# Kernel optimization log

Measured on AMD Instinct MI355X. Metric: run time of the kernel, lower is better.

## Reference

```python
import jax, jax.numpy as jnp
import numpy as np

D_MODEL = 512
NHEAD = 8
DIM = D_MODEL // NHEAD
EPS_ATT = 1e-6
EPS_LN = 1e-5


def layer_norm(x, gamma, beta):
    mu = jnp.mean(x, axis=-1, keepdims=True)
    var = jnp.mean(jnp.square(x - mu), axis=-1, keepdims=True)
    return (x - mu) * jax.lax.rsqrt(var + EPS_LN) * gamma + beta


def setup_inputs() -> dict:
    key = jax.random.key(0)
    ks = jax.random.split(key, 12)
    B, L = 4, 4096
    s = 1.0 / np.sqrt(D_MODEL)
    inp = {
        "q": jax.random.normal(ks[0], (B, L, D_MODEL), jnp.float32),
        "k": jax.random.normal(ks[1], (B, L, D_MODEL), jnp.float32),
        "v": jax.random.normal(ks[2], (B, L, D_MODEL), jnp.float32),
        # weights stored [in, out] so application is x @ W (== torch Linear with W.T)
        "Wq": jax.random.normal(ks[3], (D_MODEL, D_MODEL), jnp.float32) * s,
        "Wk": jax.random.normal(ks[4], (D_MODEL, D_MODEL), jnp.float32) * s,
        "Wv": jax.random.normal(ks[5], (D_MODEL, D_MODEL), jnp.float32) * s,
        "Wm": jax.random.normal(ks[6], (D_MODEL, D_MODEL), jnp.float32) * s,
        "W1": jax.random.normal(ks[7], (D_MODEL, 4 * D_MODEL), jnp.float32) * s,
        "W2": jax.random.normal(ks[8], (4 * D_MODEL, D_MODEL), jnp.float32) * (0.5 * s),
        "g1": jnp.ones((D_MODEL,), jnp.float32),
        "b1": jnp.zeros((D_MODEL,), jnp.float32),
        "g2": jnp.ones((D_MODEL,), jnp.float32),
        "b2": jnp.zeros((D_MODEL,), jnp.float32),
    }
    return inp


def reference(q, k, v, Wq, Wk, Wv, Wm, W1, W2, g1, b1, g2, b2):
    B, L, _ = q.shape
    S = k.shape[1]
    # projections -> [B, L, H, D]
    Qp = (q @ Wq).reshape(B, L, NHEAD, DIM)
    Kp = (k @ Wk).reshape(B, S, NHEAD, DIM)
    Vp = (v @ Wv).reshape(B, S, NHEAD, DIM)
    # elu+1 feature map linear attention
    Q = jax.nn.elu(Qp) + 1.0
    K = jax.nn.elu(Kp) + 1.0
    Vn = Vp / S
    KV = jnp.einsum('nshd,nshv->nhdv', K, Vn)          # [B,H,D,D]
    Z = 1.0 / (jnp.einsum('nlhd,nhd->nlh', Q, K.sum(axis=1)) + EPS_ATT)
    msg = jnp.einsum('nlhd,nhdv,nlh->nlhv', Q, KV, Z) * S  # [B,L,H,D]
    # merge + residual + norm1
    msg = msg.reshape(B, L, D_MODEL) @ Wm
    msg = layer_norm(msg + q, g1, b1)
    # FFN; note original adds mlp output to q (not norm1 output)
    ffn = jax.nn.relu(msg @ W1) @ W2
    out = layer_norm(q + ffn, g2, b2)
    return out
```

## Files before the change

kernel.cpp:

```cpp
#include <hip/hip_runtime.h>

typedef unsigned short u16;
typedef unsigned int u32;

typedef __bf16 bf16x8 __attribute__((ext_vector_type(8)));
typedef float f32x4 __attribute__((ext_vector_type(4)));

#define EPI_BF16 0
#define EPI_ELU1 1
#define EPI_RELU 2
#define EPI_ADDRES_F32 3
#define EPI_PROJ3 4

__device__ __forceinline__ float bf2f(u16 x) {
    u32 u = ((u32)x) << 16;
    return __uint_as_float(u);
}
__device__ __forceinline__ u16 f2bf(float f) {
    u32 u = __float_as_uint(f);
    u32 r = (u + 0x7FFFu + ((u >> 16) & 1u)) >> 16;
    return (u16)r;
}

__device__ __forceinline__ void gload_lds16(const u16* g, u16* l) {
    __builtin_amdgcn_global_load_lds(
        (const __attribute__((address_space(1))) u32*)g,
        (__attribute__((address_space(3))) u32*)l, 16, 0, 0);
}

__global__ __launch_bounds__(256) void f2b3_k(
    const float* __restrict__ q, const float* __restrict__ k,
    const float* __restrict__ v, u16* __restrict__ out) {
    int bid = blockIdx.x;
    int w = bid >> 13;
    const float* in = (w == 0) ? q : (w == 1) ? k : v;
    int i = ((bid & 8191) * 256 + threadIdx.x) * 4;
    float4 f = *(const float4*)(in + i);
    ushort4 o;
    o.x = f2bf(f.x); o.y = f2bf(f.y); o.z = f2bf(f.z); o.w = f2bf(f.w);
    *(ushort4*)(out + (long)w * 8388608 + i) = o;
}

__global__ __launch_bounds__(256) void transpose4_k(
    const float* __restrict__ W0, const float* __restrict__ W1,
    const float* __restrict__ W2, const float* __restrict__ W3,
    u16* __restrict__ out) {
    int idx = blockIdx.x * 256 + threadIdx.x;
    int w = idx >> 18, local = idx & 262143;
    const float* in = (w == 0) ? W0 : (w == 1) ? W1 : (w == 2) ? W2 : W3;
    int c = local >> 9, r = local & 511;
    out[idx] = f2bf(in[r * 512 + c]);
}

__global__ __launch_bounds__(256) void transpose2_k(
    const float* __restrict__ W1, const float* __restrict__ W2,
    u16* __restrict__ out) {
    int idx = blockIdx.x * 256 + threadIdx.x;
    if (idx < 1048576) {
        int c = idx / 512, r = idx % 512;
        out[idx] = f2bf(W1[(long)r * 2048 + c]);
    } else {
        int local = idx - 1048576;
        int c = local / 2048, r = local % 2048;
        out[idx] = f2bf(W2[(long)r * 512 + c]);
    }
}

__global__ __launch_bounds__(256) void gemm_bt(
    const u16* __restrict__ A, const u16* __restrict__ Bt,
    void* __restrict__ C, const float* __restrict__ Res,
    int M, int N, int K, int epi)
{
    __shared__ __align__(16) u16 As[2][4096];
    __shared__ __align__(16) u16 Bs[2][4096];

    int t = threadIdx.x;
    int gx = gridDim.x;
    int nwg = gx * gridDim.y;
    int bid = blockIdx.y * gx + blockIdx.x;
    if ((nwg & 7) == 0) {
        int cpx = nwg >> 3;
        bid = (bid & 7) * cpx + (bid >> 3);
    }
    int m0 = (bid / gx) * 128, n0 = (bid % gx) * 128;

    int third = 0;
    if (epi == EPI_PROJ3) {
        third = n0 >> 9;
        A += (long)third * 8388608;
    }

    int wave = t >> 6, lane = t & 63;
    int wm = (wave >> 1) * 64, wn = (wave & 1) * 64;
    int lrow = lane & 15, lk8 = (lane >> 4) * 8;

    f32x4 acc[4][4] = {};

    int srow = wave * 16 + (lane >> 2);
    int scol = (lane & 3) * 8;
    const u16* pA0 = A + (long)(m0 + srow) * K + scol;
    const u16* pB0 = Bt + (long)(n0 + srow) * K + scol;
    const long s64 = (long)64 * K;

    int nt = K >> 5;
    int cur = 0;

    {
        u16* a = As[0] + wave * 512;
        u16* b = Bs[0] + wave * 512;
        gload_lds16(pA0, a);
        gload_lds16(pA0 + s64, a + 2048);
        gload_lds16(pB0, b);
        gload_lds16(pB0 + s64, b + 2048);
    }
    __builtin_amdgcn_s_waitcnt(0);
    __syncthreads();

    for (int kt = 0; kt < nt; ++kt) {
        if (kt + 1 < nt) {
            int k0 = (kt + 1) << 5;
            u16* a = As[cur ^ 1] + wave * 512;
            u16* b = Bs[cur ^ 1] + wave * 512;
            gload_lds16(pA0 + k0, a);
            gload_lds16(pA0 + s64 + k0, a + 2048);
            gload_lds16(pB0 + k0, b);
            gload_lds16(pB0 + s64 + k0, b + 2048);
        }

        const u16* As_c = As[cur];
        const u16* Bs_c = Bs[cur];
        bf16x8 af[4], bfr[4];
#pragma unroll
        for (int mi = 0; mi < 4; mi++)
            af[mi] = *(const bf16x8*)(As_c + (wm + mi * 16 + lrow) * 32 + lk8);
#pragma unroll
        for (int ni = 0; ni < 4; ni++)
            bfr[ni] = *(const bf16x8*)(Bs_c + (wn + ni * 16 + lrow) * 32 + lk8);
#pragma unroll
        for (int mi = 0; mi < 4; mi++)
#pragma unroll
            for (int ni = 0; ni < 4; ni++)
                acc[mi][ni] = __builtin_amdgcn_mfma_f32_16x16x32_bf16(
                    af[mi], bfr[ni], acc[mi][ni], 0, 0, 0);

        if (kt + 1 < nt) {
            __builtin_amdgcn_s_waitcnt(0);
            __syncthreads();
            cur ^= 1;
        }
    }

    int rq = (lane >> 4) * 4;
    int colb = n0 + wn + (lane & 15);
#pragma unroll
    for (int mi = 0; mi < 4; mi++) {
#pragma unroll
        for (int ni = 0; ni < 4; ni++) {
#pragma unroll
            for (int r = 0; r < 4; r++) {
                int row = m0 + wm + mi * 16 + rq + r;
                int col = colb + ni * 16;
                float v0 = acc[mi][ni][r];
                if (epi == EPI_PROJ3) {
                    u16* Cb = (u16*)C + (long)third * 8388608;
                    long idx = (long)row * 512 + (col - (third << 9));
                    float v = (third < 2)
                                  ? (v0 > 0.f ? v0 + 1.f : __expf(v0))
                                  : v0;
                    Cb[idx] = f2bf(v);
                } else {
                    long idx = (long)row * N + col;
                    if (epi == EPI_ELU1) {
                        float v = v0 > 0.f ? v0 + 1.f : __expf(v0);
                        ((u16*)C)[idx] = f2bf(v);
                    } else if (epi == EPI_RELU) {
                        ((u16*)C)[idx] = f2bf(v0 > 0.f ? v0 : 0.f);
                    } else if (epi == EPI_ADDRES_F32) {
                        ((float*)C)[idx] = v0 + Res[idx];
                    } else {
                        ((u16*)C)[idx] = f2bf(v0);
                    }
                }
            }
        }
    }
}

__global__ __launch_bounds__(256) void gemm_bt64(
    const u16* __restrict__ A, const u16* __restrict__ Bt,
    void* __restrict__ C, const float* __restrict__ Res,
    int M, int N, int K, int epi)
{
    __shared__ __align__(16) u16 As[2][8192];
    __shared__ __align__(16) u16 Bs[2][8192];

    int t = threadIdx.x;
    int gx = gridDim.x;
    int nwg = gx * gridDim.y;
    int bid = blockIdx.y * gx + blockIdx.x;
    if ((nwg & 7) == 0) {
        int cpx = nwg >> 3;
        bid = (bid & 7) * cpx + (bid >> 3);
    }
    int m0 = (bid / gx) * 128, n0 = (bid % gx) * 128;

    int wave = t >> 6, lane = t & 63;
    int wm = (wave >> 1) * 64, wn = (wave & 1) * 64;
    int lrow = lane & 15, lk8 = (lane >> 4) * 8;

    f32x4 acc[4][4] = {};

    int srow = wave * 16 + (lane >> 2);
    int scol = (lane & 3) * 8;
    const u16* pA0 = A + (long)(m0 + srow) * K + scol;
    const u16* pB0 = Bt + (long)(n0 + srow) * K + scol;
    const long s64 = (long)64 * K;

    int nt = K >> 6;
    int cur = 0;

    {
        u16* a = As[0] + wave * 512;
        u16* b = Bs[0] + wave * 512;
#pragma unroll
        for (int kk = 0; kk < 2; kk++) {
            gload_lds16(pA0 + kk * 32, a + kk * 4096);
            gload_lds16(pA0 + s64 + kk * 32, a + kk * 4096 + 2048);
            gload_lds16(pB0 + kk * 32, b + kk * 4096);
            gload_lds16(pB0 + s64 + kk * 32, b + kk * 4096 + 2048);
        }
    }
    __builtin_amdgcn_s_waitcnt(0);
    __syncthreads();

    for (int kt = 0; kt < nt; ++kt) {
        if (kt + 1 < nt) {
            int k0 = (kt + 1) << 6;
            u16* a = As[cur ^ 1] + wave * 512;
            u16* b = Bs[cur ^ 1] + wave * 512;
#pragma unroll
            for (int kk = 0; kk < 2; kk++) {
                gload_lds16(pA0 + k0 + kk * 32, a + kk * 4096);
                gload_lds16(pA0 + s64 + k0 + kk * 32, a + kk * 4096 + 2048);
                gload_lds16(pB0 + k0 + kk * 32, b + kk * 4096);
                gload_lds16(pB0 + s64 + k0 + kk * 32, b + kk * 4096 + 2048);
            }
        }

#pragma unroll
        for (int kk = 0; kk < 2; kk++) {
            const u16* As_c = As[cur] + kk * 4096;
            const u16* Bs_c = Bs[cur] + kk * 4096;
            bf16x8 af[4], bfr[4];
#pragma unroll
            for (int mi = 0; mi < 4; mi++)
                af[mi] = *(const bf16x8*)(As_c + (wm + mi * 16 + lrow) * 32 + lk8);
#pragma unroll
            for (int ni = 0; ni < 4; ni++)
                bfr[ni] = *(const bf16x8*)(Bs_c + (wn + ni * 16 + lrow) * 32 + lk8);
#pragma unroll
            for (int mi = 0; mi < 4; mi++)
#pragma unroll
                for (int ni = 0; ni < 4; ni++)
                    acc[mi][ni] = __builtin_amdgcn_mfma_f32_16x16x32_bf16(
                        af[mi], bfr[ni], acc[mi][ni], 0, 0, 0);
        }

        if (kt + 1 < nt) {
            __builtin_amdgcn_s_waitcnt(0);
            __syncthreads();
            cur ^= 1;
        }
    }

    int rq = (lane >> 4) * 4;
    int colb = n0 + wn + (lane & 15);
#pragma unroll
    for (int mi = 0; mi < 4; mi++) {
#pragma unroll
        for (int ni = 0; ni < 4; ni++) {
#pragma unroll
            for (int r = 0; r < 4; r++) {
                int row = m0 + wm + mi * 16 + rq + r;
                int col = colb + ni * 16;
                long idx = (long)row * N + col;
                float v0 = acc[mi][ni][r];
                if (epi == EPI_ELU1) {
                    float v = v0 > 0.f ? v0 + 1.f : __expf(v0);
                    ((u16*)C)[idx] = f2bf(v);
                } else if (epi == EPI_RELU) {
                    ((u16*)C)[idx] = f2bf(v0 > 0.f ? v0 : 0.f);
                } else if (epi == EPI_ADDRES_F32) {
                    ((float*)C)[idx] = v0 + Res[idx];
                } else {
                    ((u16*)C)[idx] = f2bf(v0);
                }
            }
        }
    }
}

__global__ __launch_bounds__(256) void kv_part(
    const u16* __restrict__ Kf, const u16* __restrict__ Vf,
    float* __restrict__ Part, float* __restrict__ KsPart)
{
    __shared__ float sKf[64 * 68];
    __shared__ float sVf[64 * 68];
    int bh = blockIdx.x;
    int b = bh >> 3, h = bh & 7;
    int t = threadIdx.x;
    int d = t & 63, vg = t >> 6;

    float acc[16] = {};
    float ks = 0.f;

    for (int st = 0; st < 2; ++st) {
        int s0 = blockIdx.y * 128 + st * 64;
        {
            int row = t >> 2, c16 = (t & 3) * 16;
            long g = ((long)b * 4096 + s0 + row) * 512 + h * 64 + c16;
            uint4 kk0 = *(const uint4*)(Kf + g);
            uint4 kk1 = *(const uint4*)(Kf + g + 8);
            uint4 vv0 = *(const uint4*)(Vf + g);
            uint4 vv1 = *(const uint4*)(Vf + g + 8);
            float* dk = sKf + row * 68 + c16;
            float* dv = sVf + row * 68 + c16;
            u32 kw[8] = {kk0.x, kk0.y, kk0.z, kk0.w, kk1.x, kk1.y, kk1.z, kk1.w};
            u32 vw[8] = {vv0.x, vv0.y, vv0.z, vv0.w, vv1.x, vv1.y, vv1.z, vv1.w};
#pragma unroll
            for (int j = 0; j < 8; j++) {
                dk[2 * j]     = __uint_as_float(kw[j] << 16);
                dk[2 * j + 1] = __uint_as_float(kw[j] & 0xFFFF0000u);
                dv[2 * j]     = __uint_as_float(vw[j] << 16);
                dv[2 * j + 1] = __uint_as_float(vw[j] & 0xFFFF0000u);
            }
        }
        __syncthreads();

#pragma unroll 4
        for (int s = 0; s < 64; s++) {
            float kd = sKf[s * 68 + d];
            if (vg == 0) ks += kd;
            const float* vr = sVf + s * 68 + vg * 16;
            float4 v0 = *(const float4*)(vr);
            float4 v1 = *(const float4*)(vr + 4);
            float4 v2 = *(const float4*)(vr + 8);
            float4 v3 = *(const float4*)(vr + 12);
            acc[0]  += kd * v0.x; acc[1]  += kd * v0.y;
            acc[2]  += kd * v0.z; acc[3]  += kd * v0.w;
            acc[4]  += kd * v1.x; acc[5]  += kd * v1.y;
            acc[6]  += kd * v1.z; acc[7]  += kd * v1.w;
            acc[8]  += kd * v2.x; acc[9]  += kd * v2.y;
            acc[10] += kd * v2.z; acc[11] += kd * v2.w;
            acc[12] += kd * v3.x; acc[13] += kd * v3.y;
            acc[14] += kd * v3.z; acc[15] += kd * v3.w;
        }
        __syncthreads();
    }

    float* pp = Part + ((long)bh * 32 + blockIdx.y) * 4096 + d * 64 + vg * 16;
#pragma unroll
    for (int j = 0; j < 16; j++) pp[j] = acc[j];
    if (vg == 0) KsPart[((bh * 32) + blockIdx.y) * 64 + d] = ks;
}

__global__ __launch_bounds__(256) void kv_reduce(
    const float* __restrict__ Part, const float* __restrict__ KsPart,
    float* __restrict__ KV, float* __restrict__ Ksum)
{
    int i = blockIdx.x * 256 + threadIdx.x;
    if (i < 131072) {
        int bh = i >> 12, dv = i & 4095;
        const float* p = Part + (long)bh * 32 * 4096 + dv;
        float s = 0.f;
#pragma unroll 8
        for (int sp = 0; sp < 32; sp++) s += p[(long)sp * 4096];
        KV[i] = s;
    } else if (i < 133120) {
        int j = i - 131072;
        int bh = j >> 6, d = j & 63;
        const float* p = KsPart + bh * 32 * 64 + d;
        float s = 0.f;
#pragma unroll 8
        for (int sp = 0; sp < 32; sp++) s += p[sp * 64];
        Ksum[j] = s;
    }
}

__global__ __launch_bounds__(256) void msg_k(
    const u16* __restrict__ Q, const float* __restrict__ KV,
    const float* __restrict__ Ksum, u16* __restrict__ Msg)
{
    __shared__ float sKVt[64 * 68];
    __shared__ float sQ[64 * 68];
    __shared__ float sKs[64];
    __shared__ float sZ[64];

    int bh = blockIdx.x;
    int b = bh >> 3, h = bh & 7;
    int l0 = blockIdx.y * 64;
    int t = threadIdx.x, wave = t >> 6, lane = t & 63;

    {
        const float* src = KV + (long)bh * 4096 + t * 16;
        int d = t >> 2;
        int v0 = (t & 3) * 16;
        float4 a0 = *(const float4*)(src);
        float4 a1 = *(const float4*)(src + 4);
        float4 a2 = *(const float4*)(src + 8);
        float4 a3 = *(const float4*)(src + 12);
        float tmp[16] = {a0.x, a0.y, a0.z, a0.w, a1.x, a1.y, a1.z, a1.w,
                         a2.x, a2.y, a2.z, a2.w, a3.x, a3.y, a3.z, a3.w};
#pragma unroll
        for (int j = 0; j < 16; j++) sKVt[(v0 + j) * 68 + d] = tmp[j];
    }
    {
        int row = t >> 2, c = (t & 3) * 16;
        const u16* src = Q + ((long)b * 4096 + l0 + row) * 512 + h * 64 + c;
        uint4 q0 = *(const uint4*)(src);
        uint4 q1 = *(const uint4*)(src + 8);
        float* dq = sQ + row * 68 + c;
        u32 qw[8] = {q0.x, q0.y, q0.z, q0.w, q1.x, q1.y, q1.z, q1.w};
#pragma unroll
        for (int j = 0; j < 8; j++) {
            dq[2 * j]     = __uint_as_float(qw[j] << 16);
            dq[2 * j + 1] = __uint_as_float(qw[j] & 0xFFFF0000u);
        }
    }
    if (t < 64) sKs[t] = Ksum[bh * 64 + t];
    __syncthreads();

    float kv[64];
    {
        const float* kr = sKVt + lane * 68;
#pragma unroll
        for (int j = 0; j < 16; j++) {
            float4 x = *(const float4*)(kr + 4 * j);
            kv[4 * j]     = x.x; kv[4 * j + 1] = x.y;
            kv[4 * j + 2] = x.z; kv[4 * j + 3] = x.w;
        }
    }
    if (t < 64) {
        const float* qr = sQ + t * 68;
        float zp = 0.f;
#pragma unroll
        for (int d = 0; d < 64; d++) zp += qr[d] * sKs[d];
        sZ[t] = 1.f / (zp + 1e-6f);
    }
    __syncthreads();

    const long obase = ((long)b * 4096 + l0) * 512 + h * 64 + lane;
    int lbase = wave * 16;
#pragma unroll 4
    for (int i = 0; i < 16; i++) {
        int ll = lbase + i;
        const float* qr = sQ + ll * 68;
        float a0 = 0.f, a1 = 0.f, a2 = 0.f, a3 = 0.f;
#pragma unroll
        for (int db = 0; db < 16; db++) {
            float4 q4 = *(const float4*)(qr + 4 * db);
            a0 += q4.x * kv[4 * db];
            a1 += q4.y * kv[4 * db + 1];
            a2 += q4.z * kv[4 * db + 2];
            a3 += q4.w * kv[4 * db + 3];
        }
        float acc = (a0 + a1) + (a2 + a3);
        Msg[obase + (long)ll * 512] = f2bf(acc * sZ[ll]);
    }
}

__global__ __launch_bounds__(256) void ln_k(
    const float* __restrict__ X, const float* __restrict__ g,
    const float* __restrict__ bta, u16* __restrict__ OutB,
    float* __restrict__ OutF, int out_f32)
{
    int row = blockIdx.x;
    const float* x = X + (long)row * 512;
    int t = threadIdx.x;
    float x0 = x[t], x1 = x[t + 256];
    float s = x0 + x1, sq = x0 * x0 + x1 * x1;
#pragma unroll
    for (int off = 32; off > 0; off >>= 1) {
        s += __shfl_xor(s, off, 64);
        sq += __shfl_xor(sq, off, 64);
    }
    __shared__ float rs[4], rq[4];
    int wave = t >> 6, lane = t & 63;
    if (lane == 0) { rs[wave] = s; rq[wave] = sq; }
    __syncthreads();
    s = rs[0] + rs[1] + rs[2] + rs[3];
    sq = rq[0] + rq[1] + rq[2] + rq[3];
    float mu = s * (1.f / 512.f);
    float var = sq * (1.f / 512.f) - mu * mu;
    float rstd = rsqrtf(var + 1e-5f);
    float y0 = (x0 - mu) * rstd * g[t] + bta[t];
    float y1 = (x1 - mu) * rstd * g[t + 256] + bta[t + 256];
    if (out_f32) {
        OutF[(long)row * 512 + t] = y0;
        OutF[(long)row * 512 + t + 256] = y1;
    } else {
        OutB[(long)row * 512 + t] = f2bf(y0);
        OutB[(long)row * 512 + t + 256] = f2bf(y1);
    }
}

extern "C" void kernel_launch(void* const* d_in, const int* in_sizes, int n_in,
                              void* d_out, int out_size, void* d_ws, size_t ws_size,
                              hipStream_t stream) {
    const float* q  = (const float*)d_in[0];
    const float* k  = (const float*)d_in[1];
    const float* v  = (const float*)d_in[2];
    const float* Wq = (const float*)d_in[3];
    const float* Wk = (const float*)d_in[4];
    const float* Wv = (const float*)d_in[5];
    const float* Wm = (const float*)d_in[6];
    const float* W1 = (const float*)d_in[7];
    const float* W2 = (const float*)d_in[8];
    const float* g1 = (const float*)d_in[9];
    const float* b1 = (const float*)d_in[10];
    const float* g2 = (const float*)d_in[11];
    const float* b2 = (const float*)d_in[12];

    char* ws = (char*)d_ws;
    u16* WTq = (u16*)(ws + 0);
    u16* W1T = (u16*)(ws + 2097152);
    u16* qc  = (u16*)(ws + 6291456);
    u16* Qb  = (u16*)(ws + 56623104);
    u16* Kb  = (u16*)(ws + 73400320);
    u16* Vb  = (u16*)(ws + 90177536);
    float* KVb = (float*)(ws + 106954752);
    float* KSb = (float*)(ws + 107479040);
    u16* Msg = (u16*)(ws + 107487232);
    float* Part = (float*)(ws + 23068672);
    float* KsPart = (float*)(ws + 6291456);
    float* xpre = (float*)(ws + 23068672);
    u16* x1  = qc;
    u16* Hid = (u16*)(ws + 56623104);

    f2b3_k<<<dim3(24576), 256, 0, stream>>>(q, k, v, qc);

    transpose4_k<<<dim3(4096), 256, 0, stream>>>(Wq, Wk, Wv, Wm, WTq);
    transpose2_k<<<dim3(8192), 256, 0, stream>>>(W1, W2, W1T);

    gemm_bt<<<dim3(12, 128), 256, 0, stream>>>(qc, WTq, Qb, nullptr, 16384, 1536, 512, EPI_PROJ3);

    kv_part<<<dim3(32, 32), 256, 0, stream>>>(Kb, Vb, Part, KsPart);
    kv_reduce<<<dim3(520), 256, 0, stream>>>(Part, KsPart, KVb, KSb);
    msg_k<<<dim3(32, 64), 256, 0, stream>>>(Qb, KVb, KSb, Msg);

    gemm_bt64<<<dim3(4, 128), 256, 0, stream>>>(Msg, (u16*)(ws + 1572864), xpre, q, 16384, 512, 512, EPI_ADDRES_F32);
    ln_k<<<dim3(16384), 256, 0, stream>>>(xpre, g1, b1, x1, nullptr, 0);

    gemm_bt<<<dim3(16, 128), 256, 0, stream>>>(x1, W1T, Hid, nullptr, 16384, 2048, 512, EPI_RELU);
    gemm_bt64<<<dim3(4, 128), 256, 0, stream>>>(Hid, (u16*)(ws + 4194304), xpre, q, 16384, 512, 2048, EPI_ADDRES_F32);
    ln_k<<<dim3(16384), 256, 0, stream>>>(xpre, g2, b2, nullptr, (float*)d_out, 1);
}
```

Baseline: 476.8 us.

## Fuse prep kernels, use MFMA in kv_part, wave-per-row LayerNorm, switch FFN1 gemm

```diff
diff --git a/kernel.cpp b/kernel.cpp
--- a/kernel.cpp
+++ b/kernel.cpp
@@ -28,41 +28,40 @@
         (__attribute__((address_space(3))) u32*)l, 16, 0, 0);
 }
 
-__global__ __launch_bounds__(256) void f2b3_k(
+__global__ __launch_bounds__(256) void prep_k(
     const float* __restrict__ q, const float* __restrict__ k,
-    const float* __restrict__ v, u16* __restrict__ out) {
+    const float* __restrict__ v,
+    const float* __restrict__ Wq, const float* __restrict__ Wk,
+    const float* __restrict__ Wv, const float* __restrict__ Wm,
+    const float* __restrict__ W1, const float* __restrict__ W2,
+    u16* __restrict__ qkv_out, u16* __restrict__ wt4_out,
+    u16* __restrict__ wt2_out)
+{
     int bid = blockIdx.x;
-    int w = bid >> 13;
-    const float* in = (w == 0) ? q : (w == 1) ? k : v;
-    int i = ((bid & 8191) * 256 + threadIdx.x) * 4;
-    float4 f = *(const float4*)(in + i);
-    ushort4 o;
-    o.x = f2bf(f.x); o.y = f2bf(f.y); o.z = f2bf(f.z); o.w = f2bf(f.w);
-    *(ushort4*)(out + (long)w * 8388608 + i) = o;
-}
-
-__global__ __launch_bounds__(256) void transpose4_k(
-    const float* __restrict__ W0, const float* __restrict__ W1,
-    const float* __restrict__ W2, const float* __restrict__ W3,
-    u16* __restrict__ out) {
-    int idx = blockIdx.x * 256 + threadIdx.x;
-    int w = idx >> 18, local = idx & 262143;
-    const float* in = (w == 0) ? W0 : (w == 1) ? W1 : (w == 2) ? W2 : W3;
-    int c = local >> 9, r = local & 511;
-    out[idx] = f2bf(in[r * 512 + c]);
-}
-
-__global__ __launch_bounds__(256) void transpose2_k(
-    const float* __restrict__ W1, const float* __restrict__ W2,
-    u16* __restrict__ out) {
-    int idx = blockIdx.x * 256 + threadIdx.x;
-    if (idx < 1048576) {
-        int c = idx / 512, r = idx % 512;
-        out[idx] = f2bf(W1[(long)r * 2048 + c]);
+    if (bid < 24576) {
+        int w = bid >> 13;
+        const float* in = (w == 0) ? q : (w == 1) ? k : v;
+        int i = ((bid & 8191) * 256 + threadIdx.x) * 4;
+        float4 f = *(const float4*)(in + i);
+        ushort4 o;
+        o.x = f2bf(f.x); o.y = f2bf(f.y); o.z = f2bf(f.z); o.w = f2bf(f.w);
+        *(ushort4*)(qkv_out + (long)w * 8388608 + i) = o;
+    } else if (bid < 28672) {
+        int idx = (bid - 24576) * 256 + threadIdx.x;
+        int w = idx >> 18, local = idx & 262143;
+        const float* in = (w == 0) ? Wq : (w == 1) ? Wk : (w == 2) ? Wv : Wm;
+        int c = local >> 9, r = local & 511;
+        wt4_out[idx] = f2bf(in[r * 512 + c]);
     } else {
-        int local = idx - 1048576;
-        int c = local / 2048, r = local % 2048;
-        out[idx] = f2bf(W2[(long)r * 512 + c]);
+        int idx = (bid - 28672) * 256 + threadIdx.x;
+        if (idx < 1048576) {
+            int c = idx / 512, r = idx % 512;
+            wt2_out[idx] = f2bf(W1[(long)r * 2048 + c]);
+        } else {
+            int local = idx - 1048576;
+            int c = local / 2048, r = local % 2048;
+            wt2_out[idx] = f2bf(W2[(long)r * 512 + c]);
+        }
     }
 }
 
@@ -304,64 +303,77 @@
     const u16* __restrict__ Kf, const u16* __restrict__ Vf,
     float* __restrict__ Part, float* __restrict__ KsPart)
 {
-    __shared__ float sKf[64 * 68];
-    __shared__ float sVf[64 * 68];
+    __shared__ __align__(16) u16 sKt[64 * 72];
+    __shared__ __align__(16) u16 sVt[64 * 72];
     int bh = blockIdx.x;
     int b = bh >> 3, h = bh & 7;
     int t = threadIdx.x;
-    int d = t & 63, vg = t >> 6;
-
-    float acc[16] = {};
+    int wave = t >> 6, lane = t & 63;
+    int dblk = (wave >> 1) * 32, vblk = (wave & 1) * 32;
+    int lrow = lane & 15, lk8 = (lane >> 4) * 8;
+
+    f32x4 acc[2][2] = {};
     float ks = 0.f;
+
+    int srow = t >> 2, c16 = (t & 3) * 16;
 
     for (int st = 0; st < 2; ++st) {
         int s0 = blockIdx.y * 128 + st * 64;
         {
-            int row = t >> 2, c16 = (t & 3) * 16;
-            long g = ((long)b * 4096 + s0 + row) * 512 + h * 64 + c16;
-            uint4 kk0 = *(const uint4*)(Kf + g);
-            uint4 kk1 = *(const uint4*)(Kf + g + 8);
-            uint4 vv0 = *(const uint4*)(Vf + g);
-            uint4 vv1 = *(const uint4*)(Vf + g + 8);
-            float* dk = sKf + row * 68 + c16;
-            float* dv = sVf + row * 68 + c16;
-            u32 kw[8] = {kk0.x, kk0.y, kk0.z, kk0.w, kk1.x, kk1.y, kk1.z, kk1.w};
-            u32 vw[8] = {vv0.x, vv0.y, vv0.z, vv0.w, vv1.x, vv1.y, vv1.z, vv1.w};
-#pragma unroll
-            for (int j = 0; j < 8; j++) {
-                dk[2 * j]     = __uint_as_float(kw[j] << 16);
-                dk[2 * j + 1] = __uint_as_float(kw[j] & 0xFFFF0000u);
-                dv[2 * j]     = __uint_as_float(vw[j] << 16);
-                dv[2 * j + 1] = __uint_as_float(vw[j] & 0xFFFF0000u);
+            long g = ((long)b * 4096 + s0 + srow) * 512 + h * 64 + c16;
+            uint4 k0 = *(const uint4*)(Kf + g);
+            uint4 k1 = *(const uint4*)(Kf + g + 8);
+            uint4 v0 = *(const uint4*)(Vf + g);
+            uint4 v1 = *(const uint4*)(Vf + g + 8);
+            u32 kw[8] = {k0.x, k0.y, k0.z, k0.w, k1.x, k1.y, k1.z, k1.w};
+            u32 vw[8] = {v0.x, v0.y, v0.z, v0.w, v1.x, v1.y, v1.z, v1.w};
+            if (st) __syncthreads();
+#pragma unroll
+            for (int j = 0; j < 16; j++) {
+                u16 kv_ = (u16)(kw[j >> 1] >> ((j & 1) * 16));
+                u16 vv_ = (u16)(vw[j >> 1] >> ((j & 1) * 16));
+                sKt[(c16 + j) * 72 + srow] = kv_;
+                sVt[(c16 + j) * 72 + srow] = vv_;
             }
         }
         __syncthreads();
 
-#pragma unroll 4
-        for (int s = 0; s < 64; s++) {
-            float kd = sKf[s * 68 + d];
-            if (vg == 0) ks += kd;
-            const float* vr = sVf + s * 68 + vg * 16;
-            float4 v0 = *(const float4*)(vr);
-            float4 v1 = *(const float4*)(vr + 4);
-            float4 v2 = *(const float4*)(vr + 8);
-            float4 v3 = *(const float4*)(vr + 12);
-            acc[0]  += kd * v0.x; acc[1]  += kd * v0.y;
-            acc[2]  += kd * v0.z; acc[3]  += kd * v0.w;
-            acc[4]  += kd * v1.x; acc[5]  += kd * v1.y;
-            acc[6]  += kd * v1.z; acc[7]  += kd * v1.w;
-            acc[8]  += kd * v2.x; acc[9]  += kd * v2.y;
-            acc[10] += kd * v2.z; acc[11] += kd * v2.w;
-            acc[12] += kd * v3.x; acc[13] += kd * v3.y;
-            acc[14] += kd * v3.z; acc[15] += kd * v3.w;
-        }
-        __syncthreads();
-    }
-
-    float* pp = Part + ((long)bh * 32 + blockIdx.y) * 4096 + d * 64 + vg * 16;
-#pragma unroll
-    for (int j = 0; j < 16; j++) pp[j] = acc[j];
-    if (vg == 0) KsPart[((bh * 32) + blockIdx.y) * 64 + d] = ks;
+#pragma unroll
+        for (int ksb = 0; ksb < 2; ++ksb) {
+            int ko = ksb * 32 + lk8;
+            bf16x8 a0 = *(const bf16x8*)(sKt + (dblk + lrow) * 72 + ko);
+            bf16x8 a1 = *(const bf16x8*)(sKt + (dblk + 16 + lrow) * 72 + ko);
+            bf16x8 b0 = *(const bf16x8*)(sVt + (vblk + lrow) * 72 + ko);
+            bf16x8 b1 = *(const bf16x8*)(sVt + (vblk + 16 + lrow) * 72 + ko);
+            acc[0][0] = __builtin_amdgcn_mfma_f32_16x16x32_bf16(a0, b0, acc[0][0], 0, 0, 0);
+            acc[0][1] = __builtin_amdgcn_mfma_f32_16x16x32_bf16(a0, b1, acc[0][1], 0, 0, 0);
+            acc[1][0] = __builtin_amdgcn_mfma_f32_16x16x32_bf16(a1, b0, acc[1][0], 0, 0, 0);
+            acc[1][1] = __builtin_amdgcn_mfma_f32_16x16x32_bf16(a1, b1, acc[1][1], 0, 0, 0);
+        }
+
+        if (t < 64) {
+            const u32* rowp = (const u32*)(sKt + t * 72);
+#pragma unroll
+            for (int c = 0; c < 32; c++) {
+                u32 w = rowp[c];
+                ks += bf2f((u16)w) + bf2f((u16)(w >> 16));
+            }
+        }
+    }
+
+    int rq = (lane >> 4) * 4;
+    float* pp = Part + ((long)bh * 32 + blockIdx.y) * 4096;
+#pragma unroll
+    for (int ti = 0; ti < 2; ti++)
+#pragma unroll
+        for (int tj = 0; tj < 2; tj++)
+#pragma unroll
+            for (int r = 0; r < 4; r++) {
+                int d = dblk + ti * 16 + rq + r;
+                int vcol = vblk + tj * 16 + (lane & 15);
+                pp[d * 64 + vcol] = acc[ti][tj][r];
+            }
+    if (t < 64) KsPart[((bh * 32) + blockIdx.y) * 64 + t] = ks;
 }
 
 __global__ __launch_bounds__(256) void kv_reduce(
@@ -474,33 +486,45 @@
     const float* __restrict__ bta, u16* __restrict__ OutB,
     float* __restrict__ OutF, int out_f32)
 {
-    int row = blockIdx.x;
-    const float* x = X + (long)row * 512;
-    int t = threadIdx.x;
-    float x0 = x[t], x1 = x[t + 256];
-    float s = x0 + x1, sq = x0 * x0 + x1 * x1;
+    int wave = threadIdx.x >> 6, lane = threadIdx.x & 63;
+    long row = (long)blockIdx.x * 4 + wave;
+    const float* x = X + row * 512 + lane * 8;
+    float4 a = *(const float4*)(x);
+    float4 c = *(const float4*)(x + 4);
+    float s = (a.x + a.y) + (a.z + a.w) + (c.x + c.y) + (c.z + c.w);
+    float sq = a.x * a.x + a.y * a.y + a.z * a.z + a.w * a.w +
+               c.x * c.x + c.y * c.y + c.z * c.z + c.w * c.w;
 #pragma unroll
     for (int off = 32; off > 0; off >>= 1) {
         s += __shfl_xor(s, off, 64);
         sq += __shfl_xor(sq, off, 64);
     }
-    __shared__ float rs[4], rq[4];
-    int wave = t >> 6, lane = t & 63;
-    if (lane == 0) { rs[wave] = s; rq[wave] = sq; }
-    __syncthreads();
-    s = rs[0] + rs[1] + rs[2] + rs[3];
-    sq = rq[0] + rq[1] + rq[2] + rq[3];
     float mu = s * (1.f / 512.f);
     float var = sq * (1.f / 512.f) - mu * mu;
     float rstd = rsqrtf(var + 1e-5f);
-    float y0 = (x0 - mu) * rstd * g[t] + bta[t];
-    float y1 = (x1 - mu) * rstd * g[t + 256] + bta[t + 256];
+    float4 g0 = *(const float4*)(g + lane * 8);
+    float4 g1 = *(const float4*)(g + lane * 8 + 4);
+    float4 b0 = *(const float4*)(bta + lane * 8);
+    float4 b1 = *(const float4*)(bta + lane * 8 + 4);
+    float y0 = (a.x - mu) * rstd * g0.x + b0.x;
+    float y1 = (a.y - mu) * rstd * g0.y + b0.y;
+    float y2 = (a.z - mu) * rstd * g0.z + b0.z;
+    float y3 = (a.w - mu) * rstd * g0.w + b0.w;
+    float y4 = (c.x - mu) * rstd * g1.x + b1.x;
+    float y5 = (c.y - mu) * rstd * g1.y + b1.y;
+    float y6 = (c.z - mu) * rstd * g1.z + b1.z;
+    float y7 = (c.w - mu) * rstd * g1.w + b1.w;
     if (out_f32) {
-        OutF[(long)row * 512 + t] = y0;
-        OutF[(long)row * 512 + t + 256] = y1;
+        float* o = OutF + row * 512 + lane * 8;
+        *(float4*)(o) = make_float4(y0, y1, y2, y3);
+        *(float4*)(o + 4) = make_float4(y4, y5, y6, y7);
     } else {
-        OutB[(long)row * 512 + t] = f2bf(y0);
-        OutB[(long)row * 512 + t + 256] = f2bf(y1);
+        u32 w0 = (u32)f2bf(y0) | ((u32)f2bf(y1) << 16);
+        u32 w1 = (u32)f2bf(y2) | ((u32)f2bf(y3) << 16);
+        u32 w2 = (u32)f2bf(y4) | ((u32)f2bf(y5) << 16);
+        u32 w3 = (u32)f2bf(y6) | ((u32)f2bf(y7) << 16);
+        uint4 o = {w0, w1, w2, w3};
+        *(uint4*)(OutB + row * 512 + lane * 8) = o;
     }
 }
 
@@ -537,10 +561,8 @@
     u16* x1  = qc;
     u16* Hid = (u16*)(ws + 56623104);
 
-    f2b3_k<<<dim3(24576), 256, 0, stream>>>(q, k, v, qc);
-
-    transpose4_k<<<dim3(4096), 256, 0, stream>>>(Wq, Wk, Wv, Wm, WTq);
-    transpose2_k<<<dim3(8192), 256, 0, stream>>>(W1, W2, W1T);
+    prep_k<<<dim3(36864), 256, 0, stream>>>(q, k, v, Wq, Wk, Wv, Wm, W1, W2,
+                                            qc, WTq, W1T);
 
     gemm_bt<<<dim3(12, 128), 256, 0, stream>>>(qc, WTq, Qb, nullptr, 16384, 1536, 512, EPI_PROJ3);
 
@@ -549,9 +571,9 @@
     msg_k<<<dim3(32, 64), 256, 0, stream>>>(Qb, KVb, KSb, Msg);
 
     gemm_bt64<<<dim3(4, 128), 256, 0, stream>>>(Msg, (u16*)(ws + 1572864), xpre, q, 16384, 512, 512, EPI_ADDRES_F32);
-    ln_k<<<dim3(16384), 256, 0, stream>>>(xpre, g1, b1, x1, nullptr, 0);
-
-    gemm_bt<<<dim3(16, 128), 256, 0, stream>>>(x1, W1T, Hid, nullptr, 16384, 2048, 512, EPI_RELU);
+    ln_k<<<dim3(4096), 256, 0, stream>>>(xpre, g1, b1, x1, nullptr, 0);
+
+    gemm_bt64<<<dim3(16, 128), 256, 0, stream>>>(x1, W1T, Hid, nullptr, 16384, 2048, 512, EPI_RELU);
     gemm_bt64<<<dim3(4, 128), 256, 0, stream>>>(Hid, (u16*)(ws + 4194304), xpre, q, 16384, 512, 2048, EPI_ADDRES_F32);
-    ln_k<<<dim3(16384), 256, 0, stream>>>(xpre, g2, b2, nullptr, (float*)d_out, 1);
-}
+    ln_k<<<dim3(4096), 256, 0, stream>>>(xpre, g2, b2, nullptr, (float*)d_out, 1);
+}
```

Result: faster. 443.2 us (-7.1%).
